# Kernel tuning notes

Measured on AMD Instinct MI355X. Metric: run time of the kernel, lower is better.

The kernel has to match this reference:

```python
import jax, jax.numpy as jnp
import numpy as np

EPS = 1e-8
K = 50
COLL_TH = 1e-10
NORM_TH = 0.99


def setup_inputs() -> dict:
    key = jax.random.key(0)
    k1, k2, k3 = jax.random.split(key, 3)
    V, F = 10002, 20000
    vertices = jax.random.normal(k1, (V, 3), dtype=jnp.float32)
    faces = jax.random.randint(k2, (F, 3), 0, V, dtype=jnp.int32)
    face_probabilities = jax.random.uniform(k3, (F,), dtype=jnp.float32)
    return {"vertices": vertices, "faces": faces, "face_probabilities": face_probabilities}


def reference(vertices, faces, face_probabilities):
    F = faces.shape[0]
    v0 = vertices[faces[:, 0]]  # [F,3]
    v1 = vertices[faces[:, 1]]
    v2 = vertices[faces[:, 2]]

    # unnormalized normals (used directly in the plane-side tests, as in the torch code)
    n_un = jnp.cross(v1 - v0, v2 - v0)                                   # [F,3]
    normals = n_un / (jnp.linalg.norm(n_un, axis=1, keepdims=True) + EPS)
    cent = (v0 + v1 + v2) / 3                                            # [F,3]

    # pairwise centroid distances (torch.cdist equivalent) -> k+1 nearest
    sq = jnp.sum(cent * cent, axis=1)
    d2 = sq[:, None] + sq[None, :] - 2.0 * (cent @ cent.T)               # [F,F]
    dist = jnp.sqrt(jnp.maximum(d2, 0.0))
    k = min(K, F - 1)
    _, nbr = jax.lax.top_k(-dist, k + 1)                                 # smallest distances
    nbr = nbr[:, 1:]                                                      # drop self, [F,k]

    nv0, nv1, nv2 = v0[nbr], v1[nbr], v2[nbr]                             # [F,k,3]
    n_nbr_un = n_un[nbr]                                                  # [F,k,3]
    normals_nbr = normals[nbr]
    cent_nbr = cent[nbr]
    faces_nbr = faces[nbr]                                                # [F,k,3]

    # coplanar branch: |n . n'| > thresh -> centroid-distance test
    ndot = jnp.abs(jnp.sum(normals[:, None, :] * normals_nbr, axis=-1))   # [F,k]
    coplanar = ndot > NORM_TH
    cop_hit = jnp.linalg.norm(cent[:, None, :] - cent_nbr, axis=-1) < COLL_TH

    # non-coplanar: triangle-plane crossing test, both directions
    dA0 = jnp.sum((nv0 - v0[:, None, :]) * n_un[:, None, :], axis=-1)     # [F,k]
    dA1 = jnp.sum((nv1 - v0[:, None, :]) * n_un[:, None, :], axis=-1)
    dA2 = jnp.sum((nv2 - v0[:, None, :]) * n_un[:, None, :], axis=-1)
    condA = (dA0 * dA1 <= 0) | (dA0 * dA2 <= 0) | (dA1 * dA2 <= 0)

    dB0 = jnp.sum((v0[:, None, :] - nv0) * n_nbr_un, axis=-1)
    dB1 = jnp.sum((v1[:, None, :] - nv0) * n_nbr_un, axis=-1)
    dB2 = jnp.sum((v2[:, None, :] - nv0) * n_nbr_un, axis=-1)
    condB = (dB0 * dB1 <= 0) | (dB0 * dB2 <= 0) | (dB1 * dB2 <= 0)

    inter = jnp.where(coplanar, cop_hit, condA & condB)                   # [F,k]

    # adjacency: |set(face) & set(nearby_face)| >= 2 (set semantics: dedupe own face)
    first = jnp.stack([
        jnp.ones((F,), dtype=bool),
        faces[:, 1] != faces[:, 0],
        (faces[:, 2] != faces[:, 0]) & (faces[:, 2] != faces[:, 1]),
    ], axis=1)                                                            # [F,3]
    eq = faces[:, None, :, None] == faces_nbr[:, :, None, :]              # [F,k,3,3]
    present = jnp.any(eq, axis=-1)                                        # [F,k,3]
    shared = jnp.sum(present & first[:, None, :], axis=-1)                # [F,k]
    adjacent = shared >= 2

    collisions = inter & ~adjacent
    collision_count = jnp.sum(collisions, axis=1).astype(vertices.dtype)  # [F]
    return jnp.sum(face_probabilities * collision_count)
```

## Files before the change

### kernel.cpp

```cpp
#include <hip/hip_runtime.h>
#include <hip/hip_fp16.h>
#include <math.h>

#define WPB 4
#define RPW 4
#define EXPK 16
#define NCELL 4096
#define MAGIC 0x13579BDFu

__device__ __forceinline__ uint32_t umin32(uint32_t a, uint32_t b) { return a < b ? a : b; }
__device__ __forceinline__ uint32_t umax32(uint32_t a, uint32_t b) { return a > b ? a : b; }

__device__ __forceinline__ uint32_t expand5(uint32_t x) {
  x &= 0x1Fu;
  x = (x | (x << 8)) & 0x100Fu;
  x = (x | (x << 4)) & 0x10C3u;
  x = (x | (x << 2)) & 0x1249u;
  return x;
}
__device__ __forceinline__ uint32_t cell_of(float gx, float gy, float gz) {
  int cx = (int)((gx + 3.2f) * 2.5f);
  int cy = (int)((gy + 3.2f) * 2.5f);
  int cz = (int)((gz + 3.2f) * 2.5f);
  cx = cx < 0 ? 0 : (cx > 15 ? 15 : cx);
  cy = cy < 0 ? 0 : (cy > 15 ? 15 : cy);
  cz = cz < 0 ? 0 : (cz > 15 ? 15 : cz);
  return expand5((uint32_t)cx) | (expand5((uint32_t)cy) << 1) | (expand5((uint32_t)cz) << 2);
}

__device__ __forceinline__ void arrive_all(uint32_t* b, uint32_t n) {
  __syncthreads();
  if (threadIdx.x == 0) {
    __threadfence();
    __hip_atomic_fetch_add(b, 1u, __ATOMIC_RELEASE, __HIP_MEMORY_SCOPE_AGENT);
    while (__hip_atomic_load(b, __ATOMIC_ACQUIRE, __HIP_MEMORY_SCOPE_AGENT) < n)
      __builtin_amdgcn_s_sleep(2);
    __threadfence();
  }
  __syncthreads();
}

__global__ __launch_bounds__(256) void sortprep_kernel(
    const float* __restrict__ verts, const int* __restrict__ faces,
    const float* __restrict__ prob, float* __restrict__ out,
    uint32_t* __restrict__ bar, uint32_t* __restrict__ hist,
    uint32_t* __restrict__ perm,
    float4* __restrict__ scent, float4* __restrict__ snun,
    float4* __restrict__ sqa, float4* __restrict__ sqb, float4* __restrict__ sqc,
    ushort4* __restrict__ sfaces, float* __restrict__ sprob,
    float4* __restrict__ gcent, int F) {
  __shared__ uint32_t cbase[NCELL];
  __shared__ uint32_t wsums[4];
  const int tid = threadIdx.x;
  const int lane = tid & 63, wid = tid >> 6;
  const int f = blockIdx.x * 256 + tid;

  if (blockIdx.x == 0) {
    for (int i = tid; i < NCELL; i += 256) hist[i] = 0u;
    if (tid == 0) { bar[0] = 0u; bar[1] = 0u; out[0] = 0.0f; }
    __syncthreads();
    if (tid == 0) {
      __threadfence();
      __hip_atomic_store(&bar[7], MAGIC, __ATOMIC_RELEASE, __HIP_MEMORY_SCOPE_AGENT);
    }
  }
  if (tid == 0) {
    while (__hip_atomic_load(&bar[7], __ATOMIC_ACQUIRE, __HIP_MEMORY_SCOPE_AGENT) != MAGIC)
      __builtin_amdgcn_s_sleep(2);
  }
  __syncthreads();

  const bool valid = (f < F);
  uint32_t cell = 0, rank = 0;
  if (valid) {
    int i0 = faces[3*f+0], i1 = faces[3*f+1], i2 = faces[3*f+2];
    float gx = (verts[3*i0+0] + verts[3*i1+0] + verts[3*i2+0]) / 3.0f;
    float gy = (verts[3*i0+1] + verts[3*i1+1] + verts[3*i2+1]) / 3.0f;
    float gz = (verts[3*i0+2] + verts[3*i1+2] + verts[3*i2+2]) / 3.0f;
    cell = cell_of(gx, gy, gz);
    rank = atomicAdd(&hist[cell], 1u);
  }
  arrive_all(&bar[0], gridDim.x);

  uint32_t loc[16];
  uint32_t s = 0;
  const int base = tid * 16;
  #pragma unroll
  for (int i = 0; i < 16; ++i) { loc[i] = hist[base + i]; s += loc[i]; }
  uint32_t v = s;
  #pragma unroll
  for (int off = 1; off < 64; off <<= 1) {
    uint32_t u = (uint32_t)__shfl_up((int)v, off);
    if (lane >= off) v += u;
  }
  if (lane == 63) wsums[wid] = v;
  __syncthreads();
  if (wid == 0 && lane < 4) {
    uint32_t w = wsums[lane];
    #pragma unroll
    for (int off = 1; off < 4; off <<= 1) {
      uint32_t u = (uint32_t)__shfl_up((int)w, off);
      if (lane >= off) w += u;
    }
    wsums[lane] = w;
  }
  __syncthreads();
  uint32_t run = ((wid > 0) ? wsums[wid - 1] : 0u) + (v - s);
  #pragma unroll
  for (int i = 0; i < 16; ++i) { cbase[base + i] = run; run += loc[i]; }
  __syncthreads();

  if (valid) perm[cbase[cell] + rank] = (uint32_t)f;
  arrive_all(&bar[1], gridDim.x);

  const int slot = f;
  float gx = 0.f, gy = 0.f, gz = 0.f;
  if (slot < F) {
    int f2 = (int)perm[slot];
    int i0 = faces[3*f2+0], i1 = faces[3*f2+1], i2 = faces[3*f2+2];
    float ax = verts[3*i0+0], ay = verts[3*i0+1], az = verts[3*i0+2];
    float bx = verts[3*i1+0], by = verts[3*i1+1], bz = verts[3*i1+2];
    float cx = verts[3*i2+0], cy = verts[3*i2+1], cz = verts[3*i2+2];
    float e1x = bx-ax, e1y = by-ay, e1z = bz-az;
    float e2x = cx-ax, e2y = cy-ay, e2z = cz-az;
    float nx = e1y*e2z - e1z*e2y;
    float ny = e1z*e2x - e1x*e2z;
    float nz = e1x*e2y - e1y*e2x;
    gx = (ax+bx+cx)/3.0f; gy = (ay+by+cy)/3.0f; gz = (az+bz+cz)/3.0f;
    float sq = gx*gx + gy*gy + gz*gz;
    scent[slot] = make_float4(gx, gy, gz, sq);
    snun[slot]  = make_float4(nx, ny, nz, 0.f);
    sqa[slot]   = make_float4(ax, ay, az, 0.f);
    sqb[slot]   = make_float4(bx, by, bz, 0.f);
    sqc[slot]   = make_float4(cx, cy, cz, 0.f);
    sfaces[slot] = make_ushort4((unsigned short)i0, (unsigned short)i1, (unsigned short)i2, 0u);
    sprob[slot] = prob[f2];
  } else {
    scent[slot] = make_float4(300.f, 300.f, 300.f, 270000.f);
    float4 z = make_float4(0.f, 0.f, 0.f, 0.f);
    snun[slot] = z; sqa[slot] = z; sqb[slot] = z; sqc[slot] = z;
    sfaces[slot] = make_ushort4(0xFFFFu, 0xFFFFu, 0xFFFFu, 0u);
    sprob[slot] = 0.f;
  }
  float cnt = (slot < F) ? 1.f : 0.f;
  float mx = (slot < F) ? gx : 0.f;
  float my = (slot < F) ? gy : 0.f;
  float mz = (slot < F) ? gz : 0.f;
  #pragma unroll
  for (int m = 1; m < 16; m <<= 1) {
    mx += __shfl_xor(mx, m); my += __shfl_xor(my, m);
    mz += __shfl_xor(mz, m); cnt += __shfl_xor(cnt, m);
  }
  if ((tid & 15) == 0) {
    float4 o;
    if (cnt > 0.f) { float inv = 1.0f / cnt; o = make_float4(mx*inv, my*inv, mz*inv, cnt); }
    else o = make_float4(300.f, 300.f, 300.f, 0.f);
    gcent[slot >> 4] = o;
  }
}

__global__ __launch_bounds__(WPB * 64) void knn_collide_kernel(
    const float4* __restrict__ gcent,
    const float4* __restrict__ scent, const float4* __restrict__ snun,
    const float4* __restrict__ sqa, const float4* __restrict__ sqb,
    const float4* __restrict__ sqc, const ushort4* __restrict__ sfaces,
    const float* __restrict__ sprob,
    float* __restrict__ out, int F, int giters) {
  __shared__ float blocksum;
  __shared__ unsigned short list[WPB][RPW][64];
  const int tid = threadIdx.x;
  const int lane = tid & 63;
  const int wid = tid >> 6;
  const int rbase = (blockIdx.x * WPB + wid) * RPW;
  if (tid == 0) blocksum = 0.f;
  __syncthreads();
  const unsigned long long below = (lane == 0) ? 0ull : (~0ull >> (64 - lane));

  bool v[RPW]; int cr[RPW]; float4 ci[RPW];
  #pragma unroll
  for (int r = 0; r < RPW; ++r) {
    int rr = rbase + r;
    v[r] = (rr < F);
    cr[r] = v[r] ? rr : 0;
    ci[r] = scent[cr[r]];
  }

  uint32_t best[RPW] = {~0u, ~0u, ~0u, ~0u};
  for (int t = 0; t < giters; ++t) {
    float4 g = gcent[64*t + lane];
    uint32_t gi = (uint32_t)(64*t + lane);
    bool real = (g.w != 0.0f);
    #pragma unroll
    for (int r = 0; r < RPW; ++r) {
      float dx = g.x - ci[r].x, dy = g.y - ci[r].y, dz = g.z - ci[r].z;
      float d2 = fmaf(dz, dz, fmaf(dy, dy, dx*dx));
      uint32_t k = ((uint32_t)__half_as_ushort(__float2half_rn(d2)) << 16) | gi;
      best[r] = umin32(best[r], real ? k : ~0u);
    }
  }
  #pragma unroll
  for (int r = 0; r < RPW; ++r) {
    int own = cr[r] >> 4;
    if (lane == (own & 63)) best[r] = (uint32_t)own;
  }

  uint32_t e[RPW][4];
  #pragma unroll
  for (int r = 0; r < RPW; ++r) { e[r][0]=~0u; e[r][1]=~0u; e[r][2]=~0u; e[r][3]=~0u; }
  #pragma unroll
  for (int k = 0; k < EXPK; ++k) {
    int gslot = 4*k + (lane >> 4);
    #pragma unroll
    for (int r = 0; r < RPW; ++r) {
      int gid = 16 * (__shfl((int)best[r], gslot) & 0xFFFF) + (lane & 15);
      float4 cj = scent[gid];
      float dot = fmaf(ci[r].x, cj.x, fmaf(ci[r].y, cj.y, ci[r].z * cj.z));
      float d2 = fmaxf(fmaf(-2.0f, dot, ci[r].w + cj.w), 0.0f);
      uint32_t key = ((uint32_t)__half_as_ushort(__float2half_rn(d2)) << 16)
                     | (uint32_t)gid;
      if (gid >= F) key = ~0u;
      uint32_t c_ = key, t_;
      t_ = umin32(c_, e[r][0]); c_ = umax32(c_, e[r][0]); e[r][0] = t_;
      t_ = umin32(c_, e[r][1]); c_ = umax32(c_, e[r][1]); e[r][1] = t_;
      t_ = umin32(c_, e[r][2]); c_ = umax32(c_, e[r][2]); e[r][2] = t_;
      e[r][3] = umin32(c_, e[r][3]);
    }
  }

  uint32_t T[RPW] = {0, 0, 0, 0};
  #pragma unroll 1
  for (int bit = 14; bit >= 0; --bit) {
    #pragma unroll
    for (int r = 0; r < RPW; ++r) {
      uint32_t M = (T[r] | (1u << bit)) << 16;
      int c = __popcll(__ballot(e[r][0] < M)) + __popcll(__ballot(e[r][1] < M)) +
              __popcll(__ballot(e[r][2] < M)) + __popcll(__ballot(e[r][3] < M));
      if (c < 51) T[r] |= (1u << bit);
    }
  }

  int n[RPW];
  #pragma unroll
  for (int r = 0; r < RPW; ++r) {
    const uint32_t lim = (T[r] + 1) << 16;
    const uint32_t rw = (uint32_t)cr[r];
    bool q0 = e[r][0] < lim && (e[r][0] & 0xFFFFu) != rw;
    bool q1 = e[r][1] < lim && (e[r][1] & 0xFFFFu) != rw;
    bool q2 = e[r][2] < lim && (e[r][2] & 0xFFFFu) != rw;
    bool q3 = e[r][3] < lim && (e[r][3] & 0xFFFFu) != rw;
    unsigned long long f0 = __ballot(q0), f1 = __ballot(q1);
    unsigned long long f2 = __ballot(q2), f3 = __ballot(q3);
    int c0 = __popcll(f0);
    int c01 = c0 + __popcll(f1);
    int c012 = c01 + __popcll(f2);
    n[r] = c012 + __popcll(f3);
    int s0 = __popcll(f0 & below);
    int s1 = c0 + __popcll(f1 & below);
    int s2 = c01 + __popcll(f2 & below);
    int s3 = c012 + __popcll(f3 & below);
    if (q0 && s0 < 64) list[wid][r][s0] = (unsigned short)(e[r][0] & 0xFFFFu);
    if (q1 && s1 < 64) list[wid][r][s1] = (unsigned short)(e[r][1] & 0xFFFFu);
    if (q2 && s2 < 64) list[wid][r][s2] = (unsigned short)(e[r][2] & 0xFFFFu);
    if (q3 && s3 < 64) list[wid][r][s3] = (unsigned short)(e[r][3] & 0xFFFFu);
  }

  float wsum = 0.f;
  #pragma unroll
  for (int r = 0; r < RPW; ++r) {
    const int nr = n[r] < 64 ? n[r] : 64;
    const bool act = v[r] && (lane < nr);
    const int row = cr[r];
    const int j = (lane < nr) ? (int)list[wid][r][lane] : row;
    const float4 nui = snun[row];
    const float4 ai  = sqa[row];
    const float4 bi  = sqb[row];
    const float4 civ = sqc[row];
    const ushort4 fi = sfaces[row];
    const float4 nuj = snun[j];
    const float4 cj  = scent[j];
    const float4 aj  = sqa[j];
    const float4 bj  = sqb[j];
    const float4 cjv = sqc[j];
    const ushort4 gj = sfaces[j];
    const float4 ci_ = ci[r];
    float inv_i = 1.0f / (sqrtf(nui.x*nui.x + nui.y*nui.y + nui.z*nui.z) + 1e-8f);
    float inv_j = 1.0f / (sqrtf(nuj.x*nuj.x + nuj.y*nuj.y + nuj.z*nuj.z) + 1e-8f);
    float ndot = fabsf(nui.x*nuj.x + nui.y*nuj.y + nui.z*nuj.z) * inv_i * inv_j;
    float dx = ci_.x - cj.x, dy = ci_.y - cj.y, dz = ci_.z - cj.z;
    bool cop_hit = sqrtf(dx*dx + dy*dy + dz*dz) < 1e-10f;
    float dA0 = (aj.x-ai.x)*nui.x + (aj.y-ai.y)*nui.y + (aj.z-ai.z)*nui.z;
    float dA1 = (bj.x-ai.x)*nui.x + (bj.y-ai.y)*nui.y + (bj.z-ai.z)*nui.z;
    float dA2 = (cjv.x-ai.x)*nui.x + (cjv.y-ai.y)*nui.y + (cjv.z-ai.z)*nui.z;
    bool condA = (dA0*dA1 <= 0.f) || (dA0*dA2 <= 0.f) || (dA1*dA2 <= 0.f);
    float dB0 = (ai.x-aj.x)*nuj.x + (ai.y-aj.y)*nuj.y + (ai.z-aj.z)*nuj.z;
    float dB1 = (bi.x-aj.x)*nuj.x + (bi.y-aj.y)*nuj.y + (bi.z-aj.z)*nuj.z;
    float dB2 = (civ.x-aj.x)*nuj.x + (civ.y-aj.y)*nuj.y + (civ.z-aj.z)*nuj.z;
    bool condB = (dB0*dB1 <= 0.f) || (dB0*dB2 <= 0.f) || (dB1*dB2 <= 0.f);
    bool inter = (ndot > 0.99f) ? cop_hit : (condA && condB);
    int g0 = gj.x, g1 = gj.y, g2 = gj.z;
    int fi0 = fi.x, fi1 = fi.y, fi2 = fi.z;
    bool first1 = (fi1 != fi0), first2 = (fi2 != fi0) && (fi2 != fi1);
    int shared_ = 0;
    shared_ += ((fi0==g0) | (fi0==g1) | (fi0==g2)) ? 1 : 0;
    shared_ += (first1 && ((fi1==g0) | (fi1==g1) | (fi1==g2))) ? 1 : 0;
    shared_ += (first2 && ((fi2==g0) | (fi2==g1) | (fi2==g2))) ? 1 : 0;
    bool coll = act && inter && (shared_ < 2);
    unsigned long long cm = __ballot(coll);
    if (lane == 0 && v[r]) wsum += sprob[row] * (float)__popcll(cm);
  }
  if (lane == 0) atomicAdd(&blocksum, wsum);
  __syncthreads();
  if (tid == 0) atomicAdd(out, blocksum);
}

extern "C" void kernel_launch(void* const* d_in, const int* in_sizes, int n_in,
                              void* d_out, int out_size, void* d_ws, size_t ws_size,
                              hipStream_t stream) {
  const float* verts = (const float*)d_in[0];
  const int*   faces = (const int*)d_in[1];
  const float* prob  = (const float*)d_in[2];
  float* out = (float*)d_out;
  int F = in_sizes[1] / 3;
  int Fpad = (F + 2047) & ~2047;
  const int ngroups = Fpad / 16;
  const int giters = ngroups / 64;
  const int pblocks = Fpad / 256;

  char* ws = (char*)d_ws;
  uint32_t* bar    = (uint32_t*)ws;                       ws += 32;
  uint32_t* hist   = (uint32_t*)ws;                       ws += NCELL * 4;
  uint32_t* perm   = (uint32_t*)ws;                       ws += (size_t)Fpad * 4;
  float4* gcent = (float4*)ws;                            ws += (size_t)ngroups * 16;
  float4* scent = (float4*)ws;                            ws += (size_t)Fpad * 16;
  float4* snun  = (float4*)ws;                            ws += (size_t)Fpad * 16;
  float4* sqa   = (float4*)ws;                            ws += (size_t)Fpad * 16;
  float4* sqb   = (float4*)ws;                            ws += (size_t)Fpad * 16;
  float4* sqc   = (float4*)ws;                            ws += (size_t)Fpad * 16;
  ushort4* sfaces = (ushort4*)ws;                         ws += (size_t)Fpad * 8;
  float* sprob  = (float*)ws;                             ws += (size_t)Fpad * 4;

  sortprep_kernel<<<pblocks, 256, 0, stream>>>(
      verts, faces, prob, out, bar, hist, perm,
      scent, snun, sqa, sqb, sqc, sfaces, sprob, gcent, F);

  int rows_per_block = WPB * RPW;
  int blocks = (F + rows_per_block - 1) / rows_per_block;
  knn_collide_kernel<<<blocks, WPB * 64, 0, stream>>>(
      gcent, scent, snun, sqa, sqb, sqc, sfaces, sprob, out, F, giters);
}
```

Baseline: 133.5 us.

## Scatter sorted face data directly and drop the permutation pass and barrier

The prep kernel now keeps each face's vertices, centroid and normal in registers and writes them straight to their bucket-sorted slot. This removes the intermediate permutation array, the second grid-wide barrier and the re-gather of faces and vertices. Group centroids are built with float atomics into per-group sums, and the KNN kernel turns them into means by multiplying by 1/16. That is only correct when every group is full, and padding slots are no longer filled with sentinel values. Per-row normal, face indices and probability are also loaded once up front in the collide kernel instead of inside the per-row loop.

```diff
diff --git a/kernel.cpp b/kernel.cpp
--- a/kernel.cpp
+++ b/kernel.cpp
@@ -44,11 +44,10 @@
     const float* __restrict__ verts, const int* __restrict__ faces,
     const float* __restrict__ prob, float* __restrict__ out,
     uint32_t* __restrict__ bar, uint32_t* __restrict__ hist,
-    uint32_t* __restrict__ perm,
     float4* __restrict__ scent, float4* __restrict__ snun,
     float4* __restrict__ sqa, float4* __restrict__ sqb, float4* __restrict__ sqc,
     ushort4* __restrict__ sfaces, float* __restrict__ sprob,
-    float4* __restrict__ gcent, int F) {
+    float4* __restrict__ gcentsum, int F, int ngroups) {
   __shared__ uint32_t cbase[NCELL];
   __shared__ uint32_t wsums[4];
   const int tid = threadIdx.x;
@@ -57,7 +56,9 @@
 
   if (blockIdx.x == 0) {
     for (int i = tid; i < NCELL; i += 256) hist[i] = 0u;
-    if (tid == 0) { bar[0] = 0u; bar[1] = 0u; out[0] = 0.0f; }
+    float4 z4 = make_float4(0.f, 0.f, 0.f, 0.f);
+    for (int i = tid; i < ngroups; i += 256) gcentsum[i] = z4;
+    if (tid == 0) { bar[0] = 0u; out[0] = 0.0f; }
     __syncthreads();
     if (tid == 0) {
       __threadfence();
@@ -71,12 +72,17 @@
   __syncthreads();
 
   const bool valid = (f < F);
+  int i0 = 0, i1 = 0, i2 = 0;
+  float ax=0,ay=0,az=0,bx=0,by=0,bz=0,cx=0,cy=0,cz=0;
+  float gx=0,gy=0,gz=0,sq=0;
   uint32_t cell = 0, rank = 0;
   if (valid) {
-    int i0 = faces[3*f+0], i1 = faces[3*f+1], i2 = faces[3*f+2];
-    float gx = (verts[3*i0+0] + verts[3*i1+0] + verts[3*i2+0]) / 3.0f;
-    float gy = (verts[3*i0+1] + verts[3*i1+1] + verts[3*i2+1]) / 3.0f;
-    float gz = (verts[3*i0+2] + verts[3*i1+2] + verts[3*i2+2]) / 3.0f;
+    i0 = faces[3*f+0]; i1 = faces[3*f+1]; i2 = faces[3*f+2];
+    ax = verts[3*i0+0]; ay = verts[3*i0+1]; az = verts[3*i0+2];
+    bx = verts[3*i1+0]; by = verts[3*i1+1]; bz = verts[3*i1+2];
+    cx = verts[3*i2+0]; cy = verts[3*i2+1]; cz = verts[3*i2+2];
+    gx = (ax+bx+cx)/3.0f; gy = (ay+by+cy)/3.0f; gz = (az+bz+cz)/3.0f;
+    sq = gx*gx + gy*gy + gz*gz;
     cell = cell_of(gx, gy, gz);
     rank = atomicAdd(&hist[cell], 1u);
   }
@@ -110,57 +116,30 @@
   for (int i = 0; i < 16; ++i) { cbase[base + i] = run; run += loc[i]; }
   __syncthreads();
 
-  if (valid) perm[cbase[cell] + rank] = (uint32_t)f;
-  arrive_all(&bar[1], gridDim.x);
-
-  const int slot = f;
-  float gx = 0.f, gy = 0.f, gz = 0.f;
-  if (slot < F) {
-    int f2 = (int)perm[slot];
-    int i0 = faces[3*f2+0], i1 = faces[3*f2+1], i2 = faces[3*f2+2];
-    float ax = verts[3*i0+0], ay = verts[3*i0+1], az = verts[3*i0+2];
-    float bx = verts[3*i1+0], by = verts[3*i1+1], bz = verts[3*i1+2];
-    float cx = verts[3*i2+0], cy = verts[3*i2+1], cz = verts[3*i2+2];
+  if (valid) {
     float e1x = bx-ax, e1y = by-ay, e1z = bz-az;
     float e2x = cx-ax, e2y = cy-ay, e2z = cz-az;
     float nx = e1y*e2z - e1z*e2y;
     float ny = e1z*e2x - e1x*e2z;
     float nz = e1x*e2y - e1y*e2x;
-    gx = (ax+bx+cx)/3.0f; gy = (ay+by+cy)/3.0f; gz = (az+bz+cz)/3.0f;
-    float sq = gx*gx + gy*gy + gz*gz;
-    scent[slot] = make_float4(gx, gy, gz, sq);
-    snun[slot]  = make_float4(nx, ny, nz, 0.f);
-    sqa[slot]   = make_float4(ax, ay, az, 0.f);
-    sqb[slot]   = make_float4(bx, by, bz, 0.f);
-    sqc[slot]   = make_float4(cx, cy, cz, 0.f);
-    sfaces[slot] = make_ushort4((unsigned short)i0, (unsigned short)i1, (unsigned short)i2, 0u);
-    sprob[slot] = prob[f2];
-  } else {
-    scent[slot] = make_float4(300.f, 300.f, 300.f, 270000.f);
-    float4 z = make_float4(0.f, 0.f, 0.f, 0.f);
-    snun[slot] = z; sqa[slot] = z; sqb[slot] = z; sqc[slot] = z;
-    sfaces[slot] = make_ushort4(0xFFFFu, 0xFFFFu, 0xFFFFu, 0u);
-    sprob[slot] = 0.f;
-  }
-  float cnt = (slot < F) ? 1.f : 0.f;
-  float mx = (slot < F) ? gx : 0.f;
-  float my = (slot < F) ? gy : 0.f;
-  float mz = (slot < F) ? gz : 0.f;
-  #pragma unroll
-  for (int m = 1; m < 16; m <<= 1) {
-    mx += __shfl_xor(mx, m); my += __shfl_xor(my, m);
-    mz += __shfl_xor(mz, m); cnt += __shfl_xor(cnt, m);
-  }
-  if ((tid & 15) == 0) {
-    float4 o;
-    if (cnt > 0.f) { float inv = 1.0f / cnt; o = make_float4(mx*inv, my*inv, mz*inv, cnt); }
-    else o = make_float4(300.f, 300.f, 300.f, 0.f);
-    gcent[slot >> 4] = o;
+    uint32_t pos = cbase[cell] + rank;
+    scent[pos] = make_float4(gx, gy, gz, sq);
+    snun[pos]  = make_float4(nx, ny, nz, 0.f);
+    sqa[pos]   = make_float4(ax, ay, az, 0.f);
+    sqb[pos]   = make_float4(bx, by, bz, 0.f);
+    sqc[pos]   = make_float4(cx, cy, cz, 0.f);
+    sfaces[pos] = make_ushort4((unsigned short)i0, (unsigned short)i1, (unsigned short)i2, 0u);
+    sprob[pos] = prob[f];
+    float* gs = (float*)&gcentsum[pos >> 4];
+    atomicAdd(gs + 0, gx);
+    atomicAdd(gs + 1, gy);
+    atomicAdd(gs + 2, gz);
+    atomicAdd(gs + 3, 1.0f);
   }
 }
 
 __global__ __launch_bounds__(WPB * 64) void knn_collide_kernel(
-    const float4* __restrict__ gcent,
+    const float4* __restrict__ gcentsum,
     const float4* __restrict__ scent, const float4* __restrict__ snun,
     const float4* __restrict__ sqa, const float4* __restrict__ sqb,
     const float4* __restrict__ sqc, const ushort4* __restrict__ sfaces,
@@ -177,22 +156,27 @@
   const unsigned long long below = (lane == 0) ? 0ull : (~0ull >> (64 - lane));
 
   bool v[RPW]; int cr[RPW]; float4 ci[RPW];
+  float4 nui[RPW]; ushort4 fi[RPW]; float pr[RPW];
   #pragma unroll
   for (int r = 0; r < RPW; ++r) {
     int rr = rbase + r;
     v[r] = (rr < F);
     cr[r] = v[r] ? rr : 0;
     ci[r] = scent[cr[r]];
+    nui[r] = snun[cr[r]];
+    fi[r]  = sfaces[cr[r]];
+    pr[r]  = sprob[cr[r]];
   }
 
   uint32_t best[RPW] = {~0u, ~0u, ~0u, ~0u};
   for (int t = 0; t < giters; ++t) {
-    float4 g = gcent[64*t + lane];
+    float4 g = gcentsum[64*t + lane];
+    float mx = g.x * 0.0625f, my = g.y * 0.0625f, mz = g.z * 0.0625f;
     uint32_t gi = (uint32_t)(64*t + lane);
     bool real = (g.w != 0.0f);
     #pragma unroll
     for (int r = 0; r < RPW; ++r) {
-      float dx = g.x - ci[r].x, dy = g.y - ci[r].y, dz = g.z - ci[r].z;
+      float dx = mx - ci[r].x, dy = my - ci[r].y, dz = mz - ci[r].z;
       float d2 = fmaf(dz, dz, fmaf(dy, dy, dx*dx));
       uint32_t k = ((uint32_t)__half_as_ushort(__float2half_rn(d2)) << 16) | gi;
       best[r] = umin32(best[r], real ? k : ~0u);
@@ -271,11 +255,9 @@
     const bool act = v[r] && (lane < nr);
     const int row = cr[r];
     const int j = (lane < nr) ? (int)list[wid][r][lane] : row;
-    const float4 nui = snun[row];
     const float4 ai  = sqa[row];
     const float4 bi  = sqb[row];
     const float4 civ = sqc[row];
-    const ushort4 fi = sfaces[row];
     const float4 nuj = snun[j];
     const float4 cj  = scent[j];
     const float4 aj  = sqa[j];
@@ -283,14 +265,15 @@
     const float4 cjv = sqc[j];
     const ushort4 gj = sfaces[j];
     const float4 ci_ = ci[r];
-    float inv_i = 1.0f / (sqrtf(nui.x*nui.x + nui.y*nui.y + nui.z*nui.z) + 1e-8f);
+    const float4 nu = nui[r];
+    float inv_i = 1.0f / (sqrtf(nu.x*nu.x + nu.y*nu.y + nu.z*nu.z) + 1e-8f);
     float inv_j = 1.0f / (sqrtf(nuj.x*nuj.x + nuj.y*nuj.y + nuj.z*nuj.z) + 1e-8f);
-    float ndot = fabsf(nui.x*nuj.x + nui.y*nuj.y + nui.z*nuj.z) * inv_i * inv_j;
+    float ndot = fabsf(nu.x*nuj.x + nu.y*nuj.y + nu.z*nuj.z) * inv_i * inv_j;
     float dx = ci_.x - cj.x, dy = ci_.y - cj.y, dz = ci_.z - cj.z;
     bool cop_hit = sqrtf(dx*dx + dy*dy + dz*dz) < 1e-10f;
-    float dA0 = (aj.x-ai.x)*nui.x + (aj.y-ai.y)*nui.y + (aj.z-ai.z)*nui.z;
-    float dA1 = (bj.x-ai.x)*nui.x + (bj.y-ai.y)*nui.y + (bj.z-ai.z)*nui.z;
-    float dA2 = (cjv.x-ai.x)*nui.x + (cjv.y-ai.y)*nui.y + (cjv.z-ai.z)*nui.z;
+    float dA0 = (aj.x-ai.x)*nu.x + (aj.y-ai.y)*nu.y + (aj.z-ai.z)*nu.z;
+    float dA1 = (bj.x-ai.x)*nu.x + (bj.y-ai.y)*nu.y + (bj.z-ai.z)*nu.z;
+    float dA2 = (cjv.x-ai.x)*nu.x + (cjv.y-ai.y)*nu.y + (cjv.z-ai.z)*nu.z;
     bool condA = (dA0*dA1 <= 0.f) || (dA0*dA2 <= 0.f) || (dA1*dA2 <= 0.f);
     float dB0 = (ai.x-aj.x)*nuj.x + (ai.y-aj.y)*nuj.y + (ai.z-aj.z)*nuj.z;
     float dB1 = (bi.x-aj.x)*nuj.x + (bi.y-aj.y)*nuj.y + (bi.z-aj.z)*nuj.z;
@@ -298,7 +281,7 @@
     bool condB = (dB0*dB1 <= 0.f) || (dB0*dB2 <= 0.f) || (dB1*dB2 <= 0.f);
     bool inter = (ndot > 0.99f) ? cop_hit : (condA && condB);
     int g0 = gj.x, g1 = gj.y, g2 = gj.z;
-    int fi0 = fi.x, fi1 = fi.y, fi2 = fi.z;
+    int fi0 = fi[r].x, fi1 = fi[r].y, fi2 = fi[r].z;
     bool first1 = (fi1 != fi0), first2 = (fi2 != fi0) && (fi2 != fi1);
     int shared_ = 0;
     shared_ += ((fi0==g0) | (fi0==g1) | (fi0==g2)) ? 1 : 0;
@@ -306,7 +289,7 @@
     shared_ += (first2 && ((fi2==g0) | (fi2==g1) | (fi2==g2))) ? 1 : 0;
     bool coll = act && inter && (shared_ < 2);
     unsigned long long cm = __ballot(coll);
-    if (lane == 0 && v[r]) wsum += sprob[row] * (float)__popcll(cm);
+    if (lane == 0 && v[r]) wsum += pr[r] * (float)__popcll(cm);
   }
   if (lane == 0) atomicAdd(&blocksum, wsum);
   __syncthreads();
@@ -329,8 +312,7 @@
   char* ws = (char*)d_ws;
   uint32_t* bar    = (uint32_t*)ws;                       ws += 32;
   uint32_t* hist   = (uint32_t*)ws;                       ws += NCELL * 4;
-  uint32_t* perm   = (uint32_t*)ws;                       ws += (size_t)Fpad * 4;
-  float4* gcent = (float4*)ws;                            ws += (size_t)ngroups * 16;
+  float4* gcentsum = (float4*)ws;                         ws += (size_t)ngroups * 16;
   float4* scent = (float4*)ws;                            ws += (size_t)Fpad * 16;
   float4* snun  = (float4*)ws;                            ws += (size_t)Fpad * 16;
   float4* sqa   = (float4*)ws;                            ws += (size_t)Fpad * 16;
@@ -340,11 +322,11 @@
   float* sprob  = (float*)ws;                             ws += (size_t)Fpad * 4;
 
   sortprep_kernel<<<pblocks, 256, 0, stream>>>(
-      verts, faces, prob, out, bar, hist, perm,
-      scent, snun, sqa, sqb, sqc, sfaces, sprob, gcent, F);
+      verts, faces, prob, out, bar, hist,
+      scent, snun, sqa, sqb, sqc, sfaces, sprob, gcentsum, F, ngroups);
 
   int rows_per_block = WPB * RPW;
   int blocks = (F + rows_per_block - 1) / rows_per_block;
   knn_collide_kernel<<<blocks, WPB * 64, 0, stream>>>(
-      gcent, scent, snun, sqa, sqb, sqc, sfaces, sprob, out, F, giters);
-}
+      gcentsum, scent, snun, sqa, sqb, sqc, sfaces, sprob, out, F, giters);
+}
```

New measurement: 127.8 us. 1.04x faster.
